# Performance work log

Measured on AMD Instinct MI355X. Metric: run time of the kernel, lower is better.

## Reference

```python
import jax, jax.numpy as jnp
import numpy as np


def setup_inputs() -> dict:
    key = jax.random.key(0)
    k1, k2, k3 = jax.random.split(key, 3)
    B, C, N, G, D = 64, 4, 1024, 32, 3
    patches = jax.random.normal(k1, (B, C, N, G, D), dtype=jnp.float32)
    centers = jax.random.normal(k2, (B, C, N, D), dtype=jnp.float32)
    # crops_centers_idx: uniform multinomial over n_patches, one per flat batch elem
    center_idx = jax.random.randint(k3, (B * C,), 0, N)
    # crop_length ~ randint(0.25*N, 0.75*N); fixed to midpoint 512 for static shapes
    return {"patches": patches, "centers": centers, "center_idx": center_idx, "K": 512}


def reference(patches, centers, center_idx, K):
    B, C, N, G, D = patches.shape
    BF = B * C
    # flatten (b, c) -> bf, matching PatchedCloud.flatten()
    p = patches.reshape(BF, N, G, D)
    c = centers.reshape(BF, N, D)
    # gather the sampled crop center per flat batch element: [BF, D]
    q = c[jnp.arange(BF), center_idx]
    # knn_points: squared L2 distances from query to all centers, K smallest (sorted)
    d2 = jnp.sum((q[:, None, :] - c) ** 2, axis=-1)  # [BF, N]
    _, idx = jax.lax.top_k(-d2, K)                   # [BF, K], ascending distance
    b = jnp.arange(BF)[:, None]
    cropped_patches = p[b, idx]   # [BF, K, G, D]
    cropped_centers = c[b, idx]   # [BF, K, D]
    return (cropped_patches.reshape(B, C, K, G, D),
            cropped_centers.reshape(B, C, K, D))
```

## Files before the change

### kernel.cpp

```cpp
#include <hip/hip_runtime.h>
#include <hip/hip_bf16.h>

#define BFN   256
#define NPTS  1024
#define KSEL  512
#define GD    96
#define ROW4  24

__global__ __launch_bounds__(1024)
void crop_sampler_kernel(const float* __restrict__ patches,
                         const float* __restrict__ centers,
                         const int*   __restrict__ center_idx,
                         float* __restrict__ out_patches,
                         float* __restrict__ out_centers)
{
    __shared__ unsigned long long keys[NPTS];

    const int bf = blockIdx.x;
    const int t  = threadIdx.x;

    const float* cbase = centers + (size_t)bf * NPTS * 3;

    const int qi = center_idx[bf];
    const float q0 = cbase[qi * 3 + 0];
    const float q1 = cbase[qi * 3 + 1];
    const float q2 = cbase[qi * 3 + 2];

    const float c0 = cbase[t * 3 + 0];
    const float c1 = cbase[t * 3 + 1];
    const float c2 = cbase[t * 3 + 2];

    const double e0 = (double)q0 - (double)c0;
    const double e1 = (double)q1 - (double)c1;
    const double e2 = (double)q2 - (double)c2;
    const double d2 = e0 * e0 + e1 * e1 + e2 * e2;

    const unsigned long long bits = (unsigned long long)__double_as_longlong(d2);
    keys[t] = (bits & 0xFFFFFFFFFFFFFC00ull) | (unsigned long long)t;

    for (int size = 2; size <= NPTS; size <<= 1) {
        for (int stride = size >> 1; stride > 0; stride >>= 1) {
            __syncthreads();
            const int partner = t ^ stride;
            if (partner > t) {
                const bool descending = (t & size) != 0;
                unsigned long long a = keys[t];
                unsigned long long b = keys[partner];
                const bool doswap = descending ? (a < b) : (a > b);
                if (doswap) { keys[t] = b; keys[partner] = a; }
            }
        }
    }
    __syncthreads();

    float* oc = out_centers + (size_t)bf * KSEL * 3;
    for (int i = t; i < KSEL * 3; i += 1024) {
        const int k = i / 3;
        const int d = i - k * 3;
        const int idx = (int)(keys[k] & 0x3FFu);
        oc[(size_t)k * 3 + d] = cbase[(size_t)idx * 3 + d];
    }

    const float4* pbase = (const float4*)(patches + (size_t)bf * NPTS * GD);
    float4*       op    = (float4*)(out_patches + (size_t)bf * KSEL * GD);
    for (int i = t; i < KSEL * ROW4; i += 1024) {
        const int k    = i / ROW4;
        const int lane = i - k * ROW4;
        const int idx  = (int)(keys[k] & 0x3FFu);
        op[(size_t)k * ROW4 + lane] = pbase[(size_t)idx * ROW4 + lane];
    }
}

extern "C" void kernel_launch(void* const* d_in, const int* in_sizes, int n_in,
                              void* d_out, int out_size, void* d_ws, size_t ws_size,
                              hipStream_t stream)
{
    const float* patches    = (const float*)d_in[0];
    const float* centers    = (const float*)d_in[1];
    const int*   center_idx = (const int*)d_in[2];

    float* out_patches = (float*)d_out;
    float* out_centers = (float*)d_out + (size_t)BFN * KSEL * GD;

    crop_sampler_kernel<<<BFN, 1024, 0, stream>>>(patches, centers, center_idx,
                                                  out_patches, out_centers);
}
```

Before: 170.6 us.

## Split top-k selection and gather into two kernels, use shuffles in bitonic sort

The fused kernel is split in two. A selection kernel runs a register-resident bitonic sort that uses wavefront xor-shuffles for strides below 64 and LDS only for larger strides, then writes the selected indices to workspace. A separate gather kernel launches many small 256-thread blocks to copy the patch rows and centers. This spreads the memory-bound gather across all CUs instead of 256 large blocks and cuts LDS traffic and barriers in the sort. The cost is an extra launch and an index round trip through global memory.

```diff
diff --git a/kernel.cpp b/kernel.cpp
--- a/kernel.cpp
+++ b/kernel.cpp
@@ -6,68 +6,79 @@
 #define KSEL  512
 #define GD    96
 #define ROW4  24
+#define PBLK  12288
+#define CBLK  512
+
+typedef unsigned long long u64;
 
 __global__ __launch_bounds__(1024)
-void crop_sampler_kernel(const float* __restrict__ patches,
-                         const float* __restrict__ centers,
-                         const int*   __restrict__ center_idx,
-                         float* __restrict__ out_patches,
-                         float* __restrict__ out_centers)
+void sel_kernel(const float* __restrict__ centers,
+                const int*   __restrict__ center_idx,
+                int* __restrict__ out_idx)
 {
-    __shared__ unsigned long long keys[NPTS];
-
+    __shared__ u64 lds[NPTS];
     const int bf = blockIdx.x;
     const int t  = threadIdx.x;
 
     const float* cbase = centers + (size_t)bf * NPTS * 3;
-
     const int qi = center_idx[bf];
-    const float q0 = cbase[qi * 3 + 0];
-    const float q1 = cbase[qi * 3 + 1];
-    const float q2 = cbase[qi * 3 + 2];
-
-    const float c0 = cbase[t * 3 + 0];
-    const float c1 = cbase[t * 3 + 1];
-    const float c2 = cbase[t * 3 + 2];
+    const float q0 = cbase[qi * 3 + 0], q1 = cbase[qi * 3 + 1], q2 = cbase[qi * 3 + 2];
+    const float c0 = cbase[t * 3 + 0],  c1 = cbase[t * 3 + 1],  c2 = cbase[t * 3 + 2];
 
     const double e0 = (double)q0 - (double)c0;
     const double e1 = (double)q1 - (double)c1;
     const double e2 = (double)q2 - (double)c2;
     const double d2 = e0 * e0 + e1 * e1 + e2 * e2;
 
-    const unsigned long long bits = (unsigned long long)__double_as_longlong(d2);
-    keys[t] = (bits & 0xFFFFFFFFFFFFFC00ull) | (unsigned long long)t;
+    u64 key = (((u64)__double_as_longlong(d2)) & ~0x3FFull) | (u64)t;
 
     for (int size = 2; size <= NPTS; size <<= 1) {
+        const bool dir = (t & size) != 0;
         for (int stride = size >> 1; stride > 0; stride >>= 1) {
-            __syncthreads();
-            const int partner = t ^ stride;
-            if (partner > t) {
-                const bool descending = (t & size) != 0;
-                unsigned long long a = keys[t];
-                unsigned long long b = keys[partner];
-                const bool doswap = descending ? (a < b) : (a > b);
-                if (doswap) { keys[t] = b; keys[partner] = a; }
+            u64 other;
+            if (stride >= 64) {
+                __syncthreads();
+                lds[t] = key;
+                __syncthreads();
+                other = lds[t ^ stride];
+            } else {
+                other = __shfl_xor(key, stride, 64);
             }
+            const bool upper    = (t & stride) != 0;
+            const bool keep_min = (upper == dir);
+            const bool mine_lt  = key < other;
+            key = (keep_min == mine_lt) ? key : other;
         }
     }
-    __syncthreads();
 
-    float* oc = out_centers + (size_t)bf * KSEL * 3;
-    for (int i = t; i < KSEL * 3; i += 1024) {
-        const int k = i / 3;
-        const int d = i - k * 3;
-        const int idx = (int)(keys[k] & 0x3FFu);
-        oc[(size_t)k * 3 + d] = cbase[(size_t)idx * 3 + d];
-    }
+    if (t < KSEL) out_idx[bf * KSEL + t] = (int)(key & 0x3FFull);
+}
 
-    const float4* pbase = (const float4*)(patches + (size_t)bf * NPTS * GD);
-    float4*       op    = (float4*)(out_patches + (size_t)bf * KSEL * GD);
-    for (int i = t; i < KSEL * ROW4; i += 1024) {
-        const int k    = i / ROW4;
-        const int lane = i - k * ROW4;
-        const int idx  = (int)(keys[k] & 0x3FFu);
-        op[(size_t)k * ROW4 + lane] = pbase[(size_t)idx * ROW4 + lane];
+__global__ __launch_bounds__(256)
+void gather_kernel(const float* __restrict__ patches,
+                   const float* __restrict__ centers,
+                   const int*   __restrict__ idx,
+                   float* __restrict__ out_p,
+                   float* __restrict__ out_c)
+{
+    const int b = blockIdx.x;
+    const int t = threadIdx.x;
+    if (b < PBLK) {
+        const int i    = b * 256 + t;
+        const int row  = i / ROW4;
+        const int lane = i - row * ROW4;
+        const int bf   = row >> 9;
+        const int src  = idx[row];
+        const float4* pb = (const float4*)patches;
+        float4 v = pb[((size_t)bf * NPTS + src) * ROW4 + lane];
+        ((float4*)out_p)[(size_t)row * ROW4 + lane] = v;
+    } else {
+        const int r  = (b - PBLK) * 256 + t;
+        const int bf = r >> 9;
+        const int src = idx[r];
+        const float* cb = centers + ((size_t)bf * NPTS + src) * 3;
+        float* oc = out_c + (size_t)r * 3;
+        oc[0] = cb[0]; oc[1] = cb[1]; oc[2] = cb[2];
     }
 }
 
@@ -81,7 +92,9 @@
 
     float* out_patches = (float*)d_out;
     float* out_centers = (float*)d_out + (size_t)BFN * KSEL * GD;
+    int*   idx_ws      = (int*)d_ws;
 
-    crop_sampler_kernel<<<BFN, 1024, 0, stream>>>(patches, centers, center_idx,
-                                                  out_patches, out_centers);
+    sel_kernel<<<BFN, 1024, 0, stream>>>(centers, center_idx, idx_ws);
+    gather_kernel<<<PBLK + CBLK, 256, 0, stream>>>(patches, centers, idx_ws,
+                                                   out_patches, out_centers);
 }
```

Result: no change. 167.7 us (-1.7%).
